# Performance work log

Hardware: AMD Instinct MI355X
Metric: run time of the kernel (lower is better)

Reference implementation:

```python
import jax, jax.numpy as jnp
import numpy as np
import math
from jax import lax

TSCALE = 256
NUM_SAMPLE = 32
PERBIN = 3
WINDOWS = [4, 8, 16, 32, 64, 128, 192, 256]
RATIO = 0.25
B = 2
DIM = 512
H1 = 256   # hid_dim_1d
H3 = 512   # hid_dim_3d
H2 = 128   # hid_dim_2d


def _bin_mask(xmin, xmax, tscale, num_sample, perbin):
    # exact replica of BEM._get_interp1d_bin_mask (setup-time numpy)
    plen = float(xmax - xmin)
    step = plen / (num_sample * perbin - 1.0)
    samples = [xmin + step * i for i in range(num_sample * perbin)]
    cols = []
    for idx in range(num_sample):
        v = np.zeros([tscale])
        for s in samples[idx * perbin:(idx + 1) * perbin]:
            up = math.ceil(s)
            dec, down = math.modf(s)
            if 0 <= int(down) <= tscale - 1:
                v[int(down)] += 1 - dec
            if 0 <= int(up) <= tscale - 1:
                v[int(up)] += dec
        cols.append(v / perbin)
    return np.stack(cols, axis=1)  # (tscale, num_sample)


def build_sample_mask():
    mats = []
    for w in WINDOWS:
        ws = w + w * RATIO
        vecs = []
        for t in range(TSCALE):
            d = ws * 0.5
            vecs.append(_bin_mask(t - d, t + d, TSCALE, NUM_SAMPLE, PERBIN))
        mats.append(np.stack(vecs, axis=2))  # (T, N, T)
    m = np.stack(mats, axis=3).astype(np.float32)  # (T, N, T, W)
    return jnp.asarray(m.reshape(TSCALE, -1))  # (T, N*T*W)


def gn(x, g, b, groups=32, eps=1e-5):
    Bsz, C = x.shape[0], x.shape[1]
    xr = x.reshape(Bsz, groups, -1)
    mu = xr.mean(-1, keepdims=True)
    var = xr.var(-1, keepdims=True)
    xr = (xr - mu) * lax.rsqrt(var + eps)
    x = xr.reshape(x.shape)
    bshape = (1, C) + (1,) * (x.ndim - 2)
    return x * g.reshape(bshape) + b.reshape(bshape)


def conv(x, w, b, strides, padding, dn):
    y = lax.conv_general_dilated(x, w, strides, padding, dimension_numbers=dn)
    return y + b.reshape((1, -1) + (1,) * (y.ndim - 2))


def setup_inputs() -> dict:
    key = jax.random.key(0)
    ks = jax.random.split(key, 16)

    def w(k, shape, fan):
        return (jax.random.normal(k, shape) * (1.0 / np.sqrt(fan))).astype(jnp.float32)

    inp = {}
    inp['x'] = jax.random.normal(ks[0], (B, DIM, TSCALE), jnp.float32)
    inp['sample_mask'] = build_sample_mask()
    inp['c1_w'] = w(ks[1], (H1, DIM, 3), DIM * 3)
    inp['c1_b'] = jnp.zeros((H1,), jnp.float32)
    inp['gn1_g'] = jnp.ones((H1,), jnp.float32)
    inp['gn1_b'] = jnp.zeros((H1,), jnp.float32)
    inp['r3d_w'] = w(ks[2], (H3, H1, NUM_SAMPLE, 1, 1), H1 * NUM_SAMPLE)
    inp['r3d_b'] = jnp.zeros((H3,), jnp.float32)
    inp['gn3_g'] = jnp.ones((H3,), jnp.float32)
    inp['gn3_b'] = jnp.zeros((H3,), jnp.float32)
    inp['r2d_w'] = w(ks[3], (H2, H3, 1, 1), H3)
    inp['r2d_b'] = jnp.zeros((H2,), jnp.float32)
    inp['gn2_g'] = jnp.ones((H2,), jnp.float32)
    inp['gn2_b'] = jnp.zeros((H2,), jnp.float32)
    inp['s1_w'] = w(ks[4], (H2, H2, 3, 3), H2 * 9)
    inp['s1_b'] = jnp.zeros((H2,), jnp.float32)
    inp['sgn_g'] = jnp.ones((H2,), jnp.float32)
    inp['sgn_b'] = jnp.zeros((H2,), jnp.float32)
    inp['s2_w'] = w(ks[5], (1, H2, 1, 1), H2)
    inp['s2_b'] = jnp.zeros((1,), jnp.float32)
    inp['e1_w'] = w(ks[6], (H2, H2, 3, 3), H2 * 9)
    inp['e1_b'] = jnp.zeros((H2,), jnp.float32)
    inp['egn_g'] = jnp.ones((H2,), jnp.float32)
    inp['egn_b'] = jnp.zeros((H2,), jnp.float32)
    inp['e2_w'] = w(ks[7], (1, H2, 1, 1), H2)
    inp['e2_b'] = jnp.zeros((1,), jnp.float32)
    return inp


def reference(x, sample_mask, c1_w, c1_b, gn1_g, gn1_b, r3d_w, r3d_b, gn3_g, gn3_b,
              r2d_w, r2d_b, gn2_g, gn2_b, s1_w, s1_b, sgn_g, sgn_b, s2_w, s2_b,
              e1_w, e1_b, egn_g, egn_b, e2_w, e2_b):
    relu = jax.nn.relu
    W = len(WINDOWS)
    # conv_1: Unit1D(k=3, same pad) + GN + ReLU  -> (B, H1, T)
    h = relu(gn(conv(x, c1_w, c1_b, (1,), [(1, 1)], ('NCH', 'OIH', 'NCH')), gn1_g, gn1_b))
    Bsz, C, T = h.shape
    # sample: dense GEMM against sparse interp1d mask -> (B, C, N, T, W)
    samp = jnp.matmul(h, sample_mask).reshape(Bsz, C, NUM_SAMPLE, T, W)
    # reduction_layer 'fc': Conv3d over the N axis (kernel=stride=N) + GN + ReLU
    y = conv(samp, r3d_w, r3d_b, (NUM_SAMPLE, 1, 1), 'VALID', ('NCDHW', 'OIDHW', 'NCDHW'))
    y = relu(gn(y, gn3_g, gn3_b))[:, :, 0]  # squeeze depth -> (B, H3, T, W)
    f = relu(gn(conv(y, r2d_w, r2d_b, (1, 1), 'VALID', ('NCHW', 'OIHW', 'NCHW')), gn2_g, gn2_b))

    def head(w1, b1, gg, gb, w2, b2):
        t = relu(gn(conv(f, w1, b1, (1, 1), [(1, 1), (1, 1)], ('NCHW', 'OIHW', 'NCHW')), gg, gb))
        return jax.nn.sigmoid(conv(t, w2, b2, (1, 1), 'VALID', ('NCHW', 'OIHW', 'NCHW')))

    cs = head(s1_w, s1_b, sgn_g, sgn_b, s2_w, s2_b)  # (B,1,T,W)
    ce = head(e1_w, e1_b, egn_g, egn_b, e2_w, e2_b)  # (B,1,T,W)
    return jnp.concatenate([cs, ce], axis=1)  # (B,2,T,W): [start, end]
```

## Files before the change

kernel.cpp:

```cpp
#include <hip/hip_runtime.h>
#include <hip/hip_bf16.h>

typedef __hip_bfloat16 bf16;
typedef __attribute__((ext_vector_type(8))) short short8;
typedef __attribute__((ext_vector_type(4))) float f32x4;

static __device__ __forceinline__ float b2f(bf16 v) { return __bfloat162float(v); }

static __device__ __forceinline__ float ldin(const void* p, long i, int bf) {
    return bf ? b2f(((const bf16*)p)[i]) : ((const float*)p)[i];
}

__global__ void detect_k(const unsigned short* __restrict__ x16, int* __restrict__ flag) {
    __shared__ int cnt[256];
    unsigned short u = x16[threadIdx.x];
    int e = (u >> 7) & 0xFF;
    cnt[threadIdx.x] = (e >= 100 && e <= 140) ? 1 : 0;
    __syncthreads();
    for (int off = 128; off > 0; off >>= 1) {
        if (threadIdx.x < off) cnt[threadIdx.x] += cnt[threadIdx.x + off];
        __syncthreads();
    }
    if (threadIdx.x == 0) *flag = (cnt[0] > 217) ? 1 : 0;
}

__global__ void cast_bf_k(const void* __restrict__ in, bf16* __restrict__ out,
                          int n, const int* __restrict__ flagp) {
    int bf = *flagp;
    int idx = blockIdx.x * 256 + threadIdx.x;
    if (idx >= n) return;
    out[idx] = __float2bfloat16(ldin(in, idx, bf));
}

__global__ __launch_bounds__(256) void transpose_w3b_k(const void* __restrict__ w3,
                                                       bf16* __restrict__ out,
                                                       const int* __restrict__ flagp) {
    int bf = *flagp;
    int h3 = blockIdx.x;
    __shared__ bf16 t[8192];
    long base = (long)h3 * 8192;
    for (int i = threadIdx.x; i < 8192; i += 256)
        t[i] = __float2bfloat16(ldin(w3, base + i, bf));
    __syncthreads();
    for (int i = threadIdx.x; i < 8192; i += 256) {
        int n = i >> 8, c = i & 255;
        out[((long)n * 512 + h3) * 256 + c] = t[c * 32 + n];
    }
}

__global__ void cast_hT_k(const float* __restrict__ h, bf16* __restrict__ out) {
    int idx = blockIdx.x * 256 + threadIdx.x;
    if (idx >= 131072) return;
    int b = idx >> 16, r = idx & 65535;
    int tau = r >> 8, c = r & 255;
    out[idx] = __float2bfloat16(h[b * 65536 + c * 256 + tau]);
}

__global__ __launch_bounds__(256) void castT_k(const float* __restrict__ y,
                                               bf16* __restrict__ yT) {
    int p0 = blockIdx.x * 64, c0 = blockIdx.y * 64, b = blockIdx.z;
    __shared__ bf16 t[64][65];
    const float* src = y + (long)b * 1048576;
    for (int i = threadIdx.x; i < 4096; i += 256) {
        int cl = i >> 6, pl = i & 63;
        t[pl][cl] = __float2bfloat16(src[(long)(c0 + cl) * 2048 + p0 + pl]);
    }
    __syncthreads();
    bf16* dst = yT + (long)b * 1048576;
    for (int i = threadIdx.x; i < 4096; i += 256) {
        int pl = i >> 6, cl = i & 63;
        dst[(long)(p0 + pl) * 512 + c0 + cl] = t[pl][cl];
    }
}

__global__ void im2col_xb_k(const void* __restrict__ x, bf16* __restrict__ out,
                            const int* __restrict__ flagp) {
    int bf = *flagp;
    int idx = blockIdx.x * 256 + threadIdx.x;
    if (idx >= 786432) return;
    int b = idx / 393216;
    int rem = idx - b * 393216;
    int t = rem / 1536, k = rem - t * 1536;
    int c = k / 3, q = k - c * 3;
    int tt = t + q - 1;
    float v = (tt >= 0 && tt < 256) ? ldin(x, ((long)b * 512 + c) * 256 + tt, bf) : 0.f;
    out[idx] = __float2bfloat16(v);
}

__global__ void im2col_fb_k(const float* __restrict__ f, bf16* __restrict__ out) {
    int idx = blockIdx.x * 256 + threadIdx.x;
    if (idx >= 4718592) return;
    int b = idx / 2359296;
    int rem = idx - b * 2359296;
    int p = rem / 1152, k = rem - p * 1152;
    int c = k / 9, q = k - c * 9;
    int dy = q / 3, dx = q - dy * 3;
    int t = p >> 3, w = p & 7;
    int tt = t + dy - 1, ww = w + dx - 1;
    float v = (tt >= 0 && tt < 256 && ww >= 0 && ww < 8)
                  ? f[((long)b * 128 + c) * 2048 + tt * 8 + ww] : 0.f;
    out[idx] = __float2bfloat16(v);
}

template<int NT>
__global__ __launch_bounds__(256) void wgemm_mfma(
    const bf16* __restrict__ A, const bf16* __restrict__ B, float* __restrict__ C,
    const void* __restrict__ bias1, const void* __restrict__ bias2,
    int M, int K, int P, int a_div, long a_zs, const int* __restrict__ flagp)
{
    int bf = *flagp;
    int z = blockIdx.z;
    const bf16* A2 = A + (long)(z / a_div) * a_zs;
    const bf16* B2 = B + (long)(z & 1) * (long)P * K;
    float* C2 = C + (long)z * M * P;
    const void* bi = (z / a_div) ? bias2 : bias1;

    int tid = threadIdx.x;
    int wv = tid >> 6, lane = tid & 63;
    int q = lane >> 4, col = lane & 15;
    int m0 = blockIdx.y * 64 + wv * 16;
    int p0 = blockIdx.x * (16 * NT);

    f32x4 acc[NT];
    #pragma unroll
    for (int i = 0; i < NT; ++i) acc[i] = (f32x4){0.f, 0.f, 0.f, 0.f};

    const short8* Ab = (const short8*)(A2 + (long)(m0 + col) * K);
    int kch = K >> 5;
    for (int kc = 0; kc < kch; ++kc) {
        short8 af = Ab[kc * 4 + q];
        #pragma unroll
        for (int nt = 0; nt < NT; ++nt) {
            const short8* Bb = (const short8*)(B2 + (long)(p0 + nt * 16 + col) * K);
            short8 bfr = Bb[kc * 4 + q];
            acc[nt] = __builtin_amdgcn_mfma_f32_16x16x32_bf16(af, bfr, acc[nt], 0, 0, 0);
        }
    }

    float bv[4];
    #pragma unroll
    for (int r = 0; r < 4; ++r) bv[r] = ldin(bi, m0 + q * 4 + r, bf);
    #pragma unroll
    for (int nt = 0; nt < NT; ++nt)
        #pragma unroll
        for (int r = 0; r < 4; ++r)
            C2[(long)(m0 + q * 4 + r) * P + p0 + nt * 16 + col] = acc[nt][r] + bv[r];
}

__global__ __launch_bounds__(1024) void gn_relu_k(
    float* __restrict__ buf, const void* __restrict__ g, const void* __restrict__ bt,
    int C, int S, int groups, const int* __restrict__ flagp)
{
    int bf = *flagp;
    int nt = blockDim.x;
    int gid = blockIdx.x;
    int b = gid / groups, gr = gid % groups;
    int cpg = C / groups;
    long cnt = (long)cpg * S;
    float* base = buf + ((long)b * C + (long)gr * cpg) * S;
    double s = 0.0, s2 = 0.0;
    for (long i = threadIdx.x; i < cnt; i += nt) {
        float v = base[i];
        s += v; s2 += (double)v * v;
    }
    __shared__ double rs[1024], rq[1024];
    rs[threadIdx.x] = s; rq[threadIdx.x] = s2;
    __syncthreads();
    for (int off = nt >> 1; off > 0; off >>= 1) {
        if (threadIdx.x < off) { rs[threadIdx.x] += rs[threadIdx.x + off]; rq[threadIdx.x] += rq[threadIdx.x + off]; }
        __syncthreads();
    }
    double mean_d = rs[0] / (double)cnt;
    float mean = (float)mean_d;
    float var = (float)(rq[0] / (double)cnt - mean_d * mean_d);
    float rstd = rsqrtf(var + 1e-5f);
    for (long i = threadIdx.x; i < cnt; i += nt) {
        int c = gr * cpg + (int)(i / S);
        float v = (base[i] - mean) * rstd * ldin(g, c, bf) + ldin(bt, c, bf);
        base[i] = v > 0.f ? v : 0.f;
    }
}

__global__ __launch_bounds__(256) void gn_part_k(
    const float* __restrict__ buf, double* __restrict__ part,
    int C, int S, int groups, int chunks)
{
    int gi = blockIdx.x / chunks, ch = blockIdx.x % chunks;
    int b = gi / groups, gr = gi % groups;
    int cpg = C / groups;
    long cnt = (long)cpg * S;
    long clen = cnt / chunks;
    const float* base = buf + ((long)b * C + (long)gr * cpg) * S + (long)ch * clen;
    double s = 0.0, s2 = 0.0;
    for (long i = threadIdx.x; i < clen; i += 256) {
        float v = base[i];
        s += v; s2 += (double)v * v;
    }
    __shared__ double rs[256], rq[256];
    rs[threadIdx.x] = s; rq[threadIdx.x] = s2;
    __syncthreads();
    for (int off = 128; off > 0; off >>= 1) {
        if (threadIdx.x < off) { rs[threadIdx.x] += rs[threadIdx.x + off]; rq[threadIdx.x] += rq[threadIdx.x + off]; }
        __syncthreads();
    }
    if (threadIdx.x == 0) { part[blockIdx.x * 2] = rs[0]; part[blockIdx.x * 2 + 1] = rq[0]; }
}

__global__ __launch_bounds__(256) void gn_apply_k(
    float* __restrict__ buf, const double* __restrict__ part,
    const void* __restrict__ g, const void* __restrict__ bt,
    int C, int S, int groups, int chunks, const int* __restrict__ flagp)
{
    int bf = *flagp;
    int gi = blockIdx.x / chunks, ch = blockIdx.x % chunks;
    int b = gi / groups, gr = gi % groups;
    int cpg = C / groups;
    long cnt = (long)cpg * S;
    long clen = cnt / chunks;
    double s = 0.0, s2 = 0.0;
    for (int k = 0; k < chunks; ++k) {
        s += part[(gi * chunks + k) * 2];
        s2 += part[(gi * chunks + k) * 2 + 1];
    }
    double mean_d = s / (double)cnt;
    float mean = (float)mean_d;
    float var = (float)(s2 / (double)cnt - mean_d * mean_d);
    float rstd = rsqrtf(var + 1e-5f);
    float* base = buf + ((long)b * C + (long)gr * cpg) * S + (long)ch * clen;
    long off0 = (long)ch * clen;
    for (long i = threadIdx.x; i < clen; i += 256) {
        int c = gr * cpg + (int)((off0 + i) / S);
        float v = (base[i] - mean) * rstd * ldin(g, c, bf) + ldin(bt, c, bf);
        base[i] = v > 0.f ? v : 0.f;
    }
}

__global__ __launch_bounds__(384) void build_table_k(
    const void* __restrict__ mask, int* __restrict__ tabd,
    float* __restrict__ tabw, const int* __restrict__ flagp)
{
    int bf = *flagp;
    int nw = blockIdx.x;
    int w = nw >> 5, n = nw & 31;
    int tid = threadIdx.x;
    int d = tid - 165;
    float v = 0.f;
    if (d <= 165) {
        if (d < 0) v = ldin(mask, (long)(254 + d) * 65536 + ((long)n * 256 + 254) * 8 + w, bf);
        else       v = ldin(mask, (long)(1 + d) * 65536 + ((long)n * 256 + 1) * 8 + w, bf);
    }
    __shared__ unsigned char nz[384];
    nz[tid] = (v != 0.f) ? 1 : 0;
    if (tid < 6) { tabd[nw * 6 + tid] = 0; tabw[nw * 6 + tid] = 0.f; }
    __syncthreads();
    if (v != 0.f) {
        int slot = 0;
        for (int j = 0; j < tid; ++j) slot += nz[j];
        if (slot < 6) { tabd[nw * 6 + slot] = d; tabw[nw * 6 + slot] = v; }
    }
}

__global__ void build_flat_k(const int* __restrict__ tabd, const float* __restrict__ tabw,
                             float* __restrict__ tabf, int* __restrict__ cntf) {
    int w = threadIdx.x;
    if (w >= 8) return;
    float2* out = (float2*)(tabf + (long)w * 384);
    int cnt = 0;
    for (int n = 0; n < 32; ++n) {
        int base = (w * 32 + n) * 6;
        for (int k = 0; k < 6; ++k) {
            float wt = tabw[base + k];
            if (wt != 0.f) {
                int d = tabd[base + k];
                out[cnt] = make_float2(wt, __int_as_float(d * 256 + n));
                cnt++;
            }
        }
    }
    if (cnt & 1) { out[cnt] = make_float2(0.f, __int_as_float(0)); cnt++; }
    for (int k = cnt; k < 192; ++k) out[k] = make_float2(0.f, __int_as_float(0));
    cntf[w] = cnt >> 1;
}

__global__ void build_corr_k(const void* __restrict__ mask, const int* __restrict__ tabd,
                             const float* __restrict__ tabw, float* __restrict__ corrT,
                             const int* __restrict__ flagp) {
    int bf = *flagp;
    int idx = blockIdx.x * 256 + threadIdx.x;
    if (idx >= 65536) return;
    int e = idx >> 8, t = idx & 255;
    int w = e >> 5, n = e & 31;
    float mv = ldin(mask, ((long)n * 256 + t) * 8 + w, bf);
    float sub = 0.f;
    int base = e * 6;
    for (int k = 0; k < 6; ++k)
        if (tabd[base + k] == -t && tabw[base + k] != 0.f) sub += tabw[base + k];
    corrT[idx] = mv - sub;
}

__global__ __launch_bounds__(1024) void apply_y8_k(
    const bf16* __restrict__ w3b, const bf16* __restrict__ hbT,
    const float* __restrict__ tabf, const int* __restrict__ cntf,
    const float* __restrict__ corrT, float* __restrict__ y,
    const void* __restrict__ r3b, const int* __restrict__ flagp)
{
    int hp = blockIdx.x;
    int h0 = hp * 2;
    int tid = threadIdx.x;
    int t = tid & 255;
    int wg = tid >> 8;
    int w0 = wg * 2;

    int wv = tid >> 6;
    int lane = tid & 63;
    int q = lane >> 4, col = lane & 15;

    __shared__ float4 Pl[32 * 256];
    __shared__ float4 TabL[768];

    for (int i = tid; i < 768; i += 1024)
        TabL[i] = ((const float4*)tabf)[i];

    int c0 = cntf[__builtin_amdgcn_readfirstlane(w0)];
    int c1 = cntf[__builtin_amdgcn_readfirstlane(w0 + 1)];

    const short8* Bb0 = (const short8*)(hbT + (long)(wv * 32 + col) * 256);
    const short8* Bb1 = Bb0 + 512;
    int jb = wv * 32 + col;
    int b_ = wv >> 3;
    int tau0 = jb & 255;
    int tau1 = (jb + 16) & 255;

    #pragma unroll 1
    for (int half = 0; half < 2; ++half) {
        int cn0 = half * 16;
        f32x4 g00 = (f32x4){0.f,0.f,0.f,0.f}, g01 = (f32x4){0.f,0.f,0.f,0.f};
        f32x4 g10 = (f32x4){0.f,0.f,0.f,0.f}, g11 = (f32x4){0.f,0.f,0.f,0.f};
        const short8* Aa0 = (const short8*)(w3b +
            ((long)(cn0 + (col >> 1)) * 512 + h0 + (col & 1)) * 256);
        const short8* Aa1 = (const short8*)(w3b +
            ((long)(cn0 + 8 + (col >> 1)) * 512 + h0 + (col & 1)) * 256);
        #pragma unroll
        for (int kc = 0; kc < 8; ++kc) {
            short8 a0 = Aa0[kc * 4 + q];
            short8 a1 = Aa1[kc * 4 + q];
            short8 b0 = Bb0[kc * 4 + q];
            short8 b1 = Bb1[kc * 4 + q];
            g00 = __builtin_amdgcn_mfma_f32_16x16x32_bf16(a0, b0, g00, 0, 0, 0);
            g01 = __builtin_amdgcn_mfma_f32_16x16x32_bf16(a0, b1, g01, 0, 0, 0);
            g10 = __builtin_amdgcn_mfma_f32_16x16x32_bf16(a1, b0, g10, 0, 0, 0);
            g11 = __builtin_amdgcn_mfma_f32_16x16x32_bf16(a1, b1, g11, 0, 0, 0);
        }
        float* Plf = (float*)Pl;
        #pragma unroll
        for (int rh = 0; rh < 2; ++rh) {
            int nl0 = cn0 + q * 2 + rh;
            int nl1 = cn0 + 8 + q * 2 + rh;
            *(float2*)&Plf[(nl0 * 256 + tau0) * 4 + b_ * 2] = make_float2(g00[2*rh], g00[2*rh+1]);
            *(float2*)&Plf[(nl0 * 256 + tau1) * 4 + b_ * 2] = make_float2(g01[2*rh], g01[2*rh+1]);
            *(float2*)&Plf[(nl1 * 256 + tau0) * 4 + b_ * 2] = make_float2(g10[2*rh], g10[2*rh+1]);
            *(float2*)&Plf[(nl1 * 256 + tau1) * 4 + b_ * 2] = make_float2(g11[2*rh], g11[2*rh+1]);
        }
    }
    __syncthreads();

    float4 acc0 = make_float4(0.f, 0.f, 0.f, 0.f);
    float4 acc1 = make_float4(0.f, 0.f, 0.f, 0.f);

    const float* cT0 = corrT + (long)w0 * 8192 + t;
    const float* cT1 = cT0 + 8192;
    #pragma unroll 8
    for (int n = 0; n < 32; ++n) {
        float4 pz = Pl[n << 8];
        float cc0 = cT0[n * 256], cc1 = cT1[n * 256];
        acc0.x += cc0 * pz.x; acc0.y += cc0 * pz.y;
        acc0.z += cc0 * pz.z; acc0.w += cc0 * pz.w;
        acc1.x += cc1 * pz.x; acc1.y += cc1 * pz.y;
        acc1.z += cc1 * pz.z; acc1.w += cc1 * pz.w;
    }

    auto tap2 = [&](float4 e, float4& acc) {
        int pkA = __float_as_int(e.y);
        int tauA = t + (pkA >> 8);
        float wA = ((unsigned)tauA < 256u) ? e.x : 0.f;
        float4 pA = Pl[((pkA & 255) << 8) + (tauA & 255)];
        acc.x += wA * pA.x; acc.y += wA * pA.y;
        acc.z += wA * pA.z; acc.w += wA * pA.w;
        int pkB = __float_as_int(e.w);
        int tauB = t + (pkB >> 8);
        float wB = ((unsigned)tauB < 256u) ? e.z : 0.f;
        float4 pB = Pl[((pkB & 255) << 8) + (tauB & 255)];
        acc.x += wB * pB.x; acc.y += wB * pB.y;
        acc.z += wB * pB.z; acc.w += wB * pB.w;
    };
    {
        const float4* Tf = TabL + w0 * 96;
        #pragma unroll 4
        for (int k = 0; k < c0; ++k) tap2(Tf[k], acc0);
    }
    {
        const float4* Tf = TabL + (w0 + 1) * 96;
        #pragma unroll 4
        for (int k = 0; k < c1; ++k) tap2(Tf[k], acc1);
    }

    __syncthreads();

    int bf = *flagp;
    float g0 = ldin(r3b, h0, bf), g1 = ldin(r3b, h0 + 1, bf);
    float* yb = (float*)Pl;
    *(float2*)&yb[0 * 2048 + t * 8 + w0] = make_float2(acc0.x + g0, acc1.x + g0);
    *(float2*)&yb[1 * 2048 + t * 8 + w0] = make_float2(acc0.y + g1, acc1.y + g1);
    *(float2*)&yb[2 * 2048 + t * 8 + w0] = make_float2(acc0.z + g0, acc1.z + g0);
    *(float2*)&yb[3 * 2048 + t * 8 + w0] = make_float2(acc0.w + g1, acc1.w + g1);
    __syncthreads();
    for (int f = tid; f < 2048; f += 1024) {
        int c = f >> 9, r = f & 511;
        int tt = r >> 1, half = r & 1;
        float4 v = *(const float4*)&yb[c * 2048 + tt * 8 + half * 4];
        int b = c >> 1, hh = h0 + (c & 1);
        *(float4*)&y[((long)b * 512 + hh) * 2048 + tt * 8 + half * 4] = v;
    }
}

__global__ __launch_bounds__(64) void head_out_k(
    const float* __restrict__ t1s, const float* __restrict__ t1e,
    const void* __restrict__ s2w, const void* __restrict__ s2b,
    const void* __restrict__ e2w, const void* __restrict__ e2b,
    void* __restrict__ out, const int* __restrict__ flagp) {
    int bf = *flagp;
    int idx = blockIdx.x * 64 + threadIdx.x;
    if (idx >= 4096) return;
    int b = idx >> 11, p = idx & 2047;
    const float* ts = t1s + (long)b * 262144 + p;
    const float* te = t1e + (long)b * 262144 + p;
    float as = ldin(s2b, 0, bf), ae = ldin(e2b, 0, bf);
    #pragma unroll 8
    for (int c = 0; c < 128; ++c) {
        as += ldin(s2w, c, bf) * ts[(long)c * 2048];
        ae += ldin(e2w, c, bf) * te[(long)c * 2048];
    }
    float vs = 1.f / (1.f + expf(-as));
    float ve = 1.f / (1.f + expf(-ae));
    long o0 = ((long)b * 2) * 2048 + p;
    long o1 = ((long)b * 2 + 1) * 2048 + p;
    if (bf) {
        ((bf16*)out)[o0] = __float2bfloat16(vs);
        ((bf16*)out)[o1] = __float2bfloat16(ve);
    } else {
        ((float*)out)[o0] = vs;
        ((float*)out)[o1] = ve;
    }
}

extern "C" void kernel_launch(void* const* d_in, const int* in_sizes, int n_in,
                              void* d_out, int out_size, void* d_ws, size_t ws_size,
                              hipStream_t stream) {
    const void* x    = d_in[0];
    const void* mask = d_in[1];
    const void* c1w  = d_in[2];
    const void* c1b  = d_in[3];
    const void* gn1g = d_in[4];
    const void* gn1b = d_in[5];
    const void* w3   = d_in[6];
    const void* r3b  = d_in[7];
    const void* gn3g = d_in[8];
    const void* gn3b = d_in[9];
    const void* w2   = d_in[10];
    const void* r2b  = d_in[11];
    const void* gn2g = d_in[12];
    const void* gn2b = d_in[13];
    const void* s1w  = d_in[14];
    const void* s1b  = d_in[15];
    const void* sgng = d_in[16];
    const void* sgnb = d_in[17];
    const void* s2w  = d_in[18];
    const void* s2b  = d_in[19];
    const void* e1w  = d_in[20];
    const void* e1b  = d_in[21];
    const void* egng = d_in[22];
    const void* egnb = d_in[23];
    const void* e2w  = d_in[24];
    const void* e2b  = d_in[25];
    float* ws = (float*)d_ws;

    int*   flagI = (int*)(ws + 0);
    float* h     = ws + 64;
    float* c1t   = ws + 131136;
    float* w2t   = ws + 524352;
    float* s1t   = ws + 589888;
    float* corrB = ws + 884800;
    float* tabw  = ws + 950336;
    int*   tabd  = (int*)(ws + 951872);
    float* tabf  = ws + 953408;
    int*   cntf  = (int*)(ws + 956480);
    float* t1s   = ws + 986176;
    float* t1e   = ws + 1510464;
    float* f     = ws + 2034752;
    float* y     = ws + 2559040;
    float* w3reg = ws + 4656192;
    float* Pb    = ws + 8850496;
    double* gnbuf = (double*)(ws + 17239104);
    bf16*  w3b   = (bf16*)w3reg;
    bf16*  hbT   = (bf16*)(w3reg + 2097152);
    bf16*  c1wb  = (bf16*)c1t;
    bf16*  w2b   = (bf16*)w2t;
    bf16*  hwb   = (bf16*)s1t;
    bf16*  colxb = (bf16*)y;
    bf16*  fcolb = (bf16*)Pb;
    bf16*  yT    = (bf16*)(Pb + 4194304);

    dim3 blk(256);
    dim3 blkG(1024);

    detect_k<<<dim3(1), blk, 0, stream>>>((const unsigned short*)x, flagI);

    cast_bf_k<<<dim3(1536), blk, 0, stream>>>(c1w, c1wb, 393216, flagI);
    cast_bf_k<<<dim3(576),  blk, 0, stream>>>(s1w, hwb, 147456, flagI);
    cast_bf_k<<<dim3(576),  blk, 0, stream>>>(e1w, hwb + 147456, 147456, flagI);
    cast_bf_k<<<dim3(256),  blk, 0, stream>>>(w2, w2b, 65536, flagI);
    transpose_w3b_k<<<dim3(512), blk, 0, stream>>>(w3, w3b, flagI);
    build_table_k<<<dim3(256), dim3(384), 0, stream>>>(mask, tabd, tabw, flagI);
    build_flat_k<<<dim3(1), dim3(64), 0, stream>>>(tabd, tabw, tabf, cntf);
    build_corr_k<<<dim3(256), blk, 0, stream>>>(mask, tabd, tabw, corrB, flagI);

    im2col_xb_k<<<dim3(3072), blk, 0, stream>>>(x, colxb, flagI);
    wgemm_mfma<1><<<dim3(16, 4, 2), blk, 0, stream>>>(
        c1wb, colxb, h, c1b, c1b, 256, 1536, 256, 1, 0L, flagI);
    gn_relu_k<<<dim3(64), blkG, 0, stream>>>(h, gn1g, gn1b, 256, 256, 32, flagI);

    cast_hT_k<<<dim3(512), blk, 0, stream>>>(h, hbT);
    apply_y8_k<<<dim3(256), dim3(1024), 0, stream>>>(
        w3b, hbT, tabf, cntf, corrB, y, r3b, flagI);
    gn_part_k<<<dim3(512), blk, 0, stream>>>(y, gnbuf, 512, 2048, 32, 8);
    gn_apply_k<<<dim3(512), blk, 0, stream>>>(y, gnbuf, gn3g, gn3b, 512, 2048, 32, 8, flagI);

    castT_k<<<dim3(32, 8, 2), blk, 0, stream>>>(y, yT);
    wgemm_mfma<2><<<dim3(64, 2, 2), blk, 0, stream>>>(
        w2b, yT, f, r2b, r2b, 128, 512, 2048, 2, 0L, flagI);
    gn_part_k<<<dim3(256), blk, 0, stream>>>(f, gnbuf, 128, 2048, 32, 4);
    gn_apply_k<<<dim3(256), blk, 0, stream>>>(f, gnbuf, gn2g, gn2b, 128, 2048, 32, 4, flagI);

    im2col_fb_k<<<dim3(18432), blk, 0, stream>>>(f, fcolb);
    wgemm_mfma<4><<<dim3(32, 2, 4), blk, 0, stream>>>(
        hwb, fcolb, t1s, s1b, e1b, 128, 1152, 2048, 2, 147456L, flagI);
    gn_part_k<<<dim3(256), blk, 0, stream>>>(t1s, gnbuf, 128, 2048, 32, 4);
    gn_apply_k<<<dim3(256), blk, 0, stream>>>(t1s, gnbuf, sgng, sgnb, 128, 2048, 32, 4, flagI);
    gn_part_k<<<dim3(256), blk, 0, stream>>>(t1e, gnbuf, 128, 2048, 32, 4);
    gn_apply_k<<<dim3(256), blk, 0, stream>>>(t1e, gnbuf, egng, egnb, 128, 2048, 32, 4, flagI);

    head_out_k<<<dim3(64), dim3(64), 0, stream>>>(t1s, t1e, s2w, s2b, e2w, e2b, d_out, flagI);
}
```

Baseline: 422.6 us.

## Fold GroupNorm apply into downstream consumers and merge tap loops

Removes the separate in-place GroupNorm apply passes. A tiny kernel now computes per-group mean and rstd, and the normalize plus ReLU is applied on the fly inside the transpose cast, the im2col, and the output head kernels. This cuts one full read and write pass over each large intermediate. It adds redundant normalization arithmetic in the consumers, most notably 9x in the im2col. The two window tap loops in apply_y8 are also merged into one loop over the larger count, which may run past the shorter window's valid table entries unless those are zero-padded.

```diff
diff --git a/kernel.cpp b/kernel.cpp
--- a/kernel.cpp
+++ b/kernel.cpp
@@ -56,14 +56,36 @@
     out[idx] = __float2bfloat16(h[b * 65536 + c * 256 + tau]);
 }
 
-__global__ __launch_bounds__(256) void castT_k(const float* __restrict__ y,
-                                               bf16* __restrict__ yT) {
+__global__ void gn_stat_k(const double* __restrict__ part, float2* __restrict__ stats,
+                          int ngi, int chunks, long cnt) {
+    int gi = threadIdx.x + blockIdx.x * blockDim.x;
+    if (gi >= ngi) return;
+    double s = 0.0, s2 = 0.0;
+    for (int k = 0; k < chunks; ++k) {
+        s += part[(gi * chunks + k) * 2];
+        s2 += part[(gi * chunks + k) * 2 + 1];
+    }
+    double mean_d = s / (double)cnt;
+    float var = (float)(s2 / (double)cnt - mean_d * mean_d);
+    stats[gi] = make_float2((float)mean_d, rsqrtf(var + 1e-5f));
+}
+
+__global__ __launch_bounds__(256) void castT_gn_k(const float* __restrict__ y,
+                                                  bf16* __restrict__ yT,
+                                                  const float2* __restrict__ stats,
+                                                  const void* __restrict__ g,
+                                                  const void* __restrict__ bt,
+                                                  const int* __restrict__ flagp) {
+    int bf = *flagp;
     int p0 = blockIdx.x * 64, c0 = blockIdx.y * 64, b = blockIdx.z;
     __shared__ bf16 t[64][65];
     const float* src = y + (long)b * 1048576;
     for (int i = threadIdx.x; i < 4096; i += 256) {
         int cl = i >> 6, pl = i & 63;
-        t[pl][cl] = __float2bfloat16(src[(long)(c0 + cl) * 2048 + p0 + pl]);
+        int c = c0 + cl;
+        float2 st = stats[b * 32 + (c >> 4)];
+        float v = (src[(long)c * 2048 + p0 + pl] - st.x) * st.y * ldin(g, c, bf) + ldin(bt, c, bf);
+        t[pl][cl] = __float2bfloat16(v > 0.f ? v : 0.f);
     }
     __syncthreads();
     bf16* dst = yT + (long)b * 1048576;
@@ -87,7 +109,11 @@
     out[idx] = __float2bfloat16(v);
 }
 
-__global__ void im2col_fb_k(const float* __restrict__ f, bf16* __restrict__ out) {
+__global__ void im2col_fb_gn_k(const float* __restrict__ f, bf16* __restrict__ out,
+                               const float2* __restrict__ stats,
+                               const void* __restrict__ g, const void* __restrict__ bt,
+                               const int* __restrict__ flagp) {
+    int bf = *flagp;
     int idx = blockIdx.x * 256 + threadIdx.x;
     if (idx >= 4718592) return;
     int b = idx / 2359296;
@@ -97,8 +123,12 @@
     int dy = q / 3, dx = q - dy * 3;
     int t = p >> 3, w = p & 7;
     int tt = t + dy - 1, ww = w + dx - 1;
-    float v = (tt >= 0 && tt < 256 && ww >= 0 && ww < 8)
-                  ? f[((long)b * 128 + c) * 2048 + tt * 8 + ww] : 0.f;
+    float v = 0.f;
+    if (tt >= 0 && tt < 256 && ww >= 0 && ww < 8) {
+        float2 st = stats[b * 32 + (c >> 2)];
+        v = (f[((long)b * 128 + c) * 2048 + tt * 8 + ww] - st.x) * st.y * ldin(g, c, bf) + ldin(bt, c, bf);
+        v = v > 0.f ? v : 0.f;
+    }
     out[idx] = __float2bfloat16(v);
 }
 
@@ -204,35 +234,6 @@
         __syncthreads();
     }
     if (threadIdx.x == 0) { part[blockIdx.x * 2] = rs[0]; part[blockIdx.x * 2 + 1] = rq[0]; }
-}
-
-__global__ __launch_bounds__(256) void gn_apply_k(
-    float* __restrict__ buf, const double* __restrict__ part,
-    const void* __restrict__ g, const void* __restrict__ bt,
-    int C, int S, int groups, int chunks, const int* __restrict__ flagp)
-{
-    int bf = *flagp;
-    int gi = blockIdx.x / chunks, ch = blockIdx.x % chunks;
-    int b = gi / groups, gr = gi % groups;
-    int cpg = C / groups;
-    long cnt = (long)cpg * S;
-    long clen = cnt / chunks;
-    double s = 0.0, s2 = 0.0;
-    for (int k = 0; k < chunks; ++k) {
-        s += part[(gi * chunks + k) * 2];
-        s2 += part[(gi * chunks + k) * 2 + 1];
-    }
-    double mean_d = s / (double)cnt;
-    float mean = (float)mean_d;
-    float var = (float)(s2 / (double)cnt - mean_d * mean_d);
-    float rstd = rsqrtf(var + 1e-5f);
-    float* base = buf + ((long)b * C + (long)gr * cpg) * S + (long)ch * clen;
-    long off0 = (long)ch * clen;
-    for (long i = threadIdx.x; i < clen; i += 256) {
-        int c = gr * cpg + (int)((off0 + i) / S);
-        float v = (base[i] - mean) * rstd * ldin(g, c, bf) + ldin(bt, c, bf);
-        base[i] = v > 0.f ? v : 0.f;
-    }
 }
 
 __global__ __launch_bounds__(384) void build_table_k(
@@ -323,6 +324,7 @@
 
     int c0 = cntf[__builtin_amdgcn_readfirstlane(w0)];
     int c1 = cntf[__builtin_amdgcn_readfirstlane(w0 + 1)];
+    int cm = c0 > c1 ? c0 : c1;
 
     const short8* Bb0 = (const short8*)(hbT + (long)(wv * 32 + col) * 256);
     const short8* Bb1 = Bb0 + 512;
@@ -394,14 +396,10 @@
         acc.z += wB * pB.z; acc.w += wB * pB.w;
     };
     {
-        const float4* Tf = TabL + w0 * 96;
+        const float4* Tf0 = TabL + w0 * 96;
+        const float4* Tf1 = Tf0 + 96;
         #pragma unroll 4
-        for (int k = 0; k < c0; ++k) tap2(Tf[k], acc0);
-    }
-    {
-        const float4* Tf = TabL + (w0 + 1) * 96;
-        #pragma unroll 4
-        for (int k = 0; k < c1; ++k) tap2(Tf[k], acc1);
+        for (int k = 0; k < cm; ++k) { tap2(Tf0[k], acc0); tap2(Tf1[k], acc1); }
     }
 
     __syncthreads();
@@ -423,8 +421,11 @@
     }
 }
 
-__global__ __launch_bounds__(64) void head_out_k(
+__global__ __launch_bounds__(64) void head_out_gn_k(
     const float* __restrict__ t1s, const float* __restrict__ t1e,
+    const float2* __restrict__ statsS, const float2* __restrict__ statsE,
+    const void* __restrict__ sgng, const void* __restrict__ sgnb,
+    const void* __restrict__ egng, const void* __restrict__ egnb,
     const void* __restrict__ s2w, const void* __restrict__ s2b,
     const void* __restrict__ e2w, const void* __restrict__ e2b,
     void* __restrict__ out, const int* __restrict__ flagp) {
@@ -435,10 +436,16 @@
     const float* ts = t1s + (long)b * 262144 + p;
     const float* te = t1e + (long)b * 262144 + p;
     float as = ldin(s2b, 0, bf), ae = ldin(e2b, 0, bf);
-    #pragma unroll 8
+    #pragma unroll 4
     for (int c = 0; c < 128; ++c) {
-        as += ldin(s2w, c, bf) * ts[(long)c * 2048];
-        ae += ldin(e2w, c, bf) * te[(long)c * 2048];
+        float2 ss = statsS[b * 32 + (c >> 2)];
+        float tv = (ts[(long)c * 2048] - ss.x) * ss.y * ldin(sgng, c, bf) + ldin(sgnb, c, bf);
+        tv = tv > 0.f ? tv : 0.f;
+        as += ldin(s2w, c, bf) * tv;
+        float2 se = statsE[b * 32 + (c >> 2)];
+        float ev = (te[(long)c * 2048] - se.x) * se.y * ldin(egng, c, bf) + ldin(egnb, c, bf);
+        ev = ev > 0.f ? ev : 0.f;
+        ae += ldin(e2w, c, bf) * ev;
     }
     float vs = 1.f / (1.f + expf(-as));
     float ve = 1.f / (1.f + expf(-ae));
@@ -494,6 +501,10 @@
     int*   tabd  = (int*)(ws + 951872);
     float* tabf  = ws + 953408;
     int*   cntf  = (int*)(ws + 956480);
+    float2* stats3 = (float2*)(ws + 956544);
+    float2* stats2 = (float2*)(ws + 956672);
+    float2* statsS = (float2*)(ws + 956800);
+    float2* statsE = (float2*)(ws + 956928);
     float* t1s   = ws + 986176;
     float* t1e   = ws + 1510464;
     float* f     = ws + 2034752;
@@ -532,22 +543,25 @@
     cast_hT_k<<<dim3(512), blk, 0, stream>>>(h, hbT);
     apply_y8_k<<<dim3(256), dim3(1024), 0, stream>>>(
         w3b, hbT, tabf, cntf, corrB, y, r3b, flagI);
+
     gn_part_k<<<dim3(512), blk, 0, stream>>>(y, gnbuf, 512, 2048, 32, 8);
-    gn_apply_k<<<dim3(512), blk, 0, stream>>>(y, gnbuf, gn3g, gn3b, 512, 2048, 32, 8, flagI);
-
-    castT_k<<<dim3(32, 8, 2), blk, 0, stream>>>(y, yT);
+    gn_stat_k<<<dim3(1), dim3(64), 0, stream>>>(gnbuf, stats3, 64, 8, 32768L);
+    castT_gn_k<<<dim3(32, 8, 2), blk, 0, stream>>>(y, yT, stats3, gn3g, gn3b, flagI);
+
     wgemm_mfma<2><<<dim3(64, 2, 2), blk, 0, stream>>>(
         w2b, yT, f, r2b, r2b, 128, 512, 2048, 2, 0L, flagI);
     gn_part_k<<<dim3(256), blk, 0, stream>>>(f, gnbuf, 128, 2048, 32, 4);
-    gn_apply_k<<<dim3(256), blk, 0, stream>>>(f, gnbuf, gn2g, gn2b, 128, 2048, 32, 4, flagI);
-
-    im2col_fb_k<<<dim3(18432), blk, 0, stream>>>(f, fcolb);
+    gn_stat_k<<<dim3(1), dim3(64), 0, stream>>>(gnbuf, stats2, 64, 4, 8192L);
+    im2col_fb_gn_k<<<dim3(18432), blk, 0, stream>>>(f, fcolb, stats2, gn2g, gn2b, flagI);
+
     wgemm_mfma<4><<<dim3(32, 2, 4), blk, 0, stream>>>(
         hwb, fcolb, t1s, s1b, e1b, 128, 1152, 2048, 2, 147456L, flagI);
     gn_part_k<<<dim3(256), blk, 0, stream>>>(t1s, gnbuf, 128, 2048, 32, 4);
-    gn_apply_k<<<dim3(256), blk, 0, stream>>>(t1s, gnbuf, sgng, sgnb, 128, 2048, 32, 4, flagI);
-    gn_part_k<<<dim3(256), blk, 0, stream>>>(t1e, gnbuf, 128, 2048, 32, 4);
-    gn_apply_k<<<dim3(256), blk, 0, stream>>>(t1e, gnbuf, egng, egnb, 128, 2048, 32, 4, flagI);
-
-    head_out_k<<<dim3(64), dim3(64), 0, stream>>>(t1s, t1e, s2w, s2b, e2w, e2b, d_out, flagI);
-}
+    gn_stat_k<<<dim3(1), dim3(64), 0, stream>>>(gnbuf, statsS, 64, 4, 8192L);
+    gn_part_k<<<dim3(256), blk, 0, stream>>>(t1e, gnbuf + 512, 128, 2048, 32, 4);
+    gn_stat_k<<<dim3(1), dim3(64), 0, stream>>>(gnbuf + 512, statsE, 64, 4, 8192L);
+
+    head_out_gn_k<<<dim3(64), dim3(64), 0, stream>>>(
+        t1s, t1e, statsS, statsE, sgng, sgnb, egng, egnb,
+        s2w, s2b, e2w, e2b, d_out, flagI);
+}
```

Measured after the change: 442.0 us. 4.6% more time.
